# Kernel tuning notes

Hardware: AMD Instinct MI355X
Metric: run time of the kernel (lower is better)

Reference implementation:

```python
import jax, jax.numpy as jnp
import numpy as np

DIM = 1024
HEADS = 16
HEAD_DIM = DIM // HEADS
HIDDEN = 4 * DIM
EPS = 1e-5


def layer_norm(x, g, b):
    mu = jnp.mean(x, axis=-1, keepdims=True)
    var = jnp.var(x, axis=-1, keepdims=True)
    return (x - mu) * jax.lax.rsqrt(var + EPS) * g + b


def setup_inputs() -> dict:
    key = jax.random.key(0)
    ks = jax.random.split(key, 8)
    B, N, C = 2, 2048, DIM
    # xavier-uniform-ish scales
    s_qkv = float(np.sqrt(6.0 / (C + 3 * C)))
    s_proj = float(np.sqrt(6.0 / (C + C)))
    s_fc1 = float(np.sqrt(6.0 / (C + HIDDEN)))
    return {
        "x": jax.random.normal(ks[0], (B, N, C), jnp.float32),
        "w_qkv": jax.random.uniform(ks[1], (3 * C, C), jnp.float32, -s_qkv, s_qkv),
        "w_proj": jax.random.uniform(ks[2], (C, C), jnp.float32, -s_proj, s_proj),
        "b_proj": jnp.zeros((C,), jnp.float32),
        "ln1_g": jnp.ones((C,), jnp.float32),
        "ln1_b": jnp.zeros((C,), jnp.float32),
        "ln2_g": jnp.ones((C,), jnp.float32),
        "ln2_b": jnp.zeros((C,), jnp.float32),
        "w_fc1": jax.random.uniform(ks[3], (HIDDEN, C), jnp.float32, -s_fc1, s_fc1),
        "b_fc1": jnp.zeros((HIDDEN,), jnp.float32),
        "w_fc2": jax.random.uniform(ks[4], (C, HIDDEN), jnp.float32, -s_fc1, s_fc1),
        "b_fc2": jnp.zeros((C,), jnp.float32),
    }


def attention(x, w_qkv, w_proj, b_proj):
    B, N, C = x.shape
    qkv = x @ w_qkv.T  # [B,N,3C]
    qkv = qkv.reshape(B, N, 3, HEADS, HEAD_DIM).transpose(2, 0, 3, 1, 4)
    q, k, v = qkv[0], qkv[1], qkv[2]  # [B,H,N,hd]
    scale = HEAD_DIM ** -0.5
    attn = jnp.einsum("bhqd,bhkd->bhqk", q, k) * scale
    attn = jax.nn.softmax(attn, axis=-1)
    out = jnp.einsum("bhqk,bhkd->bhqd", attn, v)  # [B,H,N,hd]
    out = out.transpose(0, 2, 1, 3).reshape(B, N, C)
    return out @ w_proj.T + b_proj


def reference(x, w_qkv, w_proj, b_proj, ln1_g, ln1_b, ln2_g, ln2_b, w_fc1, b_fc1, w_fc2, b_fc2):
    x = x + attention(layer_norm(x, ln1_g, ln1_b), w_qkv, w_proj, b_proj)
    h = layer_norm(x, ln2_g, ln2_b)
    h = jax.nn.gelu(h @ w_fc1.T + b_fc1, approximate=False)
    x = x + (h @ w_fc2.T + b_fc2)
    return x
```

## Files before the change

kernel.cpp:

```cpp
#include <hip/hip_runtime.h>
#include <hip/hip_bf16.h>
#include <math.h>

typedef __bf16 bf16;
typedef __attribute__((ext_vector_type(8))) __bf16 bf16x8;
typedef __attribute__((ext_vector_type(4))) __bf16 bf16x4;
typedef __attribute__((ext_vector_type(4))) float f32x4;

#define DEV static __device__ __forceinline__

typedef const void __attribute__((address_space(1)))* gptr_t;
typedef void __attribute__((address_space(3)))* lptr_t;

DEV void async16(const void* g, void* l) {
  __builtin_amdgcn_global_load_lds((gptr_t)g, (lptr_t)l, 16, 0, 0);
}

DEV void wg_barrier() {
  __builtin_amdgcn_sched_barrier(0);
  __builtin_amdgcn_s_barrier();
  __builtin_amdgcn_sched_barrier(0);
}

__global__ __launch_bounds__(256) void f2b4_kernel(const float* __restrict__ s0,
                                                   const float* __restrict__ s1,
                                                   const float* __restrict__ s2,
                                                   const float* __restrict__ s3,
                                                   bf16* __restrict__ d0, bf16* __restrict__ d1,
                                                   bf16* __restrict__ d2, bf16* __restrict__ d3,
                                                   int n0, int n1, int n2, int n3) {
  int i = (blockIdx.x * 256 + threadIdx.x) * 4;
  const float* s;
  bf16* d;
  int off;
  if (i < n0) { s = s0; d = d0; off = i; }
  else if (i < n0 + n1) { s = s1; d = d1; off = i - n0; }
  else if (i < n0 + n1 + n2) { s = s2; d = d2; off = i - n0 - n1; }
  else if (i < n0 + n1 + n2 + n3) { s = s3; d = d3; off = i - n0 - n1 - n2; }
  else return;
  float4 v = *(const float4*)(s + off);
  d[off + 0] = (bf16)v.x;
  d[off + 1] = (bf16)v.y;
  d[off + 2] = (bf16)v.z;
  d[off + 3] = (bf16)v.w;
}

__global__ __launch_bounds__(256) void ln_kernel(const float* __restrict__ in,
                                                 const float* __restrict__ g,
                                                 const float* __restrict__ b,
                                                 bf16* __restrict__ out) {
  const int row = blockIdx.x;
  const int tid = threadIdx.x;
  float4 v = ((const float4*)(in + (size_t)row * 1024))[tid];
  float s = v.x + v.y + v.z + v.w;
  float s2 = v.x * v.x + v.y * v.y + v.z * v.z + v.w * v.w;
#pragma unroll
  for (int off = 1; off < 64; off <<= 1) {
    s += __shfl_xor(s, off);
    s2 += __shfl_xor(s2, off);
  }
  __shared__ float red[8];
  int w = tid >> 6, lane = tid & 63;
  if (lane == 0) { red[w] = s; red[4 + w] = s2; }
  __syncthreads();
  s = red[0] + red[1] + red[2] + red[3];
  s2 = red[4] + red[5] + red[6] + red[7];
  const float mean = s * (1.f / 1024.f);
  const float var = s2 * (1.f / 1024.f) - mean * mean;
  const float rstd = rsqrtf(var + 1e-5f);
  float4 gv = ((const float4*)g)[tid];
  float4 bv = ((const float4*)b)[tid];
  bf16* orow = out + (size_t)row * 1024 + tid * 4;
  orow[0] = (bf16)((v.x - mean) * rstd * gv.x + bv.x);
  orow[1] = (bf16)((v.y - mean) * rstd * gv.y + bv.y);
  orow[2] = (bf16)((v.z - mean) * rstd * gv.z + bv.z);
  orow[3] = (bf16)((v.w - mean) * rstd * gv.w + bv.w);
}

template <int EPI>
__global__ __launch_bounds__(512, 2) void gemm256(const bf16* __restrict__ A,
                                                  const bf16* __restrict__ B,
                                                  bf16* __restrict__ outb,
                                                  const float* __restrict__ bias,
                                                  int M, int N, int K, int gridN) {
  __shared__ bf16 As[2][256 * 64];
  __shared__ bf16 Bs[2][256 * 64];
  const int nwg = gridDim.x;
  const int bid = blockIdx.x;
  const int swz = (bid & 7) * (nwg >> 3) + (bid >> 3);
  const int bx = swz % gridN, by = swz / gridN;
  const int brow = by * 256, bcol = bx * 256;
  const int tid = threadIdx.x;
  const int lane = tid & 63, wid = tid >> 6;
  const int wm = wid >> 2, wn = wid & 3;
  const int lr = lane & 15, lk4 = lane >> 4;
  const int strow = tid >> 3, stc = tid & 7;
  const int NT = K >> 6;
  f32x4 acc[8][4] = {};

#define STAGE(tt, bb)                                                                   \
  {                                                                                     \
    const int k0_ = (tt)*64;                                                            \
    _Pragma("unroll") for (int s_ = 0; s_ < 4; ++s_) {                                  \
      const int r_ = s_ * 64 + strow;                                                   \
      const int g_ = (stc ^ (strow & 7)) * 8;                                           \
      async16(A + (size_t)(brow + r_) * K + k0_ + g_, &As[bb][r_ * 64 + stc * 8]);      \
      async16(B + (size_t)(bcol + r_) * K + k0_ + g_, &Bs[bb][r_ * 64 + stc * 8]);      \
    }                                                                                   \
  }

  STAGE(0, 0);
  STAGE(1, 1);
  asm volatile("s_waitcnt vmcnt(8)" ::: "memory");
  wg_barrier();

  for (int t = 0; t < NT; ++t) {
    const int cur = t & 1;
    bf16x8 af[8][2], bfr[4][2];
#pragma unroll
    for (int m = 0; m < 8; ++m)
#pragma unroll
      for (int kk = 0; kk < 2; ++kk) {
        const int row = wm * 128 + m * 16 + lr;
        const int kc = kk * 4 + lk4;
        af[m][kk] = *(const bf16x8*)&As[cur][row * 64 + ((kc ^ (row & 7)) * 8)];
      }
#pragma unroll
    for (int n = 0; n < 4; ++n)
#pragma unroll
      for (int kk = 0; kk < 2; ++kk) {
        const int row = wn * 64 + n * 16 + lr;
        const int kc = kk * 4 + lk4;
        bfr[n][kk] = *(const bf16x8*)&Bs[cur][row * 64 + ((kc ^ (row & 7)) * 8)];
      }
    asm volatile("s_waitcnt lgkmcnt(0)" ::: "memory");
    wg_barrier();
    if (t + 2 < NT) STAGE(t + 2, cur);
    __builtin_amdgcn_s_setprio(1);
#pragma unroll
    for (int m = 0; m < 8; ++m)
#pragma unroll
      for (int n = 0; n < 4; ++n) {
        acc[m][n] = __builtin_amdgcn_mfma_f32_16x16x32_bf16(af[m][0], bfr[n][0], acc[m][n], 0, 0, 0);
        acc[m][n] = __builtin_amdgcn_mfma_f32_16x16x32_bf16(af[m][1], bfr[n][1], acc[m][n], 0, 0, 0);
      }
    __builtin_amdgcn_s_setprio(0);
    if (t + 1 < NT) {
      if (t + 2 < NT) {
        asm volatile("s_waitcnt vmcnt(8)" ::: "memory");
      } else {
        asm volatile("s_waitcnt vmcnt(0)" ::: "memory");
      }
      wg_barrier();
    }
  }
#undef STAGE
  const int r0 = brow + wm * 128 + lk4 * 4;
  const int c0 = bcol + wn * 64 + lr;
  float bias_v[4];
  if (EPI == 1) {
#pragma unroll
    for (int n = 0; n < 4; ++n) bias_v[n] = bias[c0 + n * 16];
  }
#pragma unroll
  for (int m = 0; m < 8; ++m)
#pragma unroll
    for (int n = 0; n < 4; ++n)
#pragma unroll
      for (int j = 0; j < 4; ++j) {
        const int r = r0 + m * 16 + j;
        const int c = c0 + n * 16;
        float v = acc[m][n][j];
        if (EPI == 1) {
          v += bias_v[n];
          v = 0.5f * v * (1.0f + erff(v * 0.70710678118654752f));
        }
        outb[(size_t)r * N + c] = (bf16)v;
      }
}

__global__ __launch_bounds__(512, 2) void gemm128(const bf16* __restrict__ A,
                                                  const bf16* __restrict__ B,
                                                  float* __restrict__ outf,
                                                  const float* __restrict__ bias,
                                                  const float* __restrict__ resid,
                                                  int M, int N, int K, int gridN) {
  __shared__ bf16 As[2][128 * 64];
  __shared__ bf16 Bs[2][128 * 64];
  const int nwg = gridDim.x;
  const int bid = blockIdx.x;
  const int swz = (bid & 7) * (nwg >> 3) + (bid >> 3);
  const int bx = swz % gridN, by = swz / gridN;
  const int brow = by * 128, bcol = bx * 128;
  const int tid = threadIdx.x;
  const int lane = tid & 63, wid = tid >> 6;
  const int wk = wid & 1, wn = (wid >> 1) & 1, wm = wid >> 2;
  const int lr = lane & 15, lk4 = lane >> 4;
  const int strow = tid >> 3, stc = tid & 7;
  const int NT = K >> 6;
  f32x4 acc[4][4] = {};

#define STAGE1(tt, bb)                                                                  \
  {                                                                                     \
    const int k0_ = (tt)*64;                                                            \
    _Pragma("unroll") for (int s_ = 0; s_ < 2; ++s_) {                                  \
      const int r_ = s_ * 64 + strow;                                                   \
      const int g_ = (stc ^ (strow & 7)) * 8;                                           \
      async16(A + (size_t)(brow + r_) * K + k0_ + g_, &As[bb][r_ * 64 + stc * 8]);      \
      async16(B + (size_t)(bcol + r_) * K + k0_ + g_, &Bs[bb][r_ * 64 + stc * 8]);      \
    }                                                                                   \
  }

  STAGE1(0, 0);
  STAGE1(1, 1);
  asm volatile("s_waitcnt vmcnt(4)" ::: "memory");
  wg_barrier();

  const int kc = wk * 4 + lk4;
  for (int t = 0; t < NT; ++t) {
    const int cur = t & 1;
    bf16x8 af[4], bfr[4];
#pragma unroll
    for (int m = 0; m < 4; ++m) {
      const int row = wm * 64 + m * 16 + lr;
      af[m] = *(const bf16x8*)&As[cur][row * 64 + ((kc ^ (row & 7)) * 8)];
    }
#pragma unroll
    for (int n = 0; n < 4; ++n) {
      const int row = wn * 64 + n * 16 + lr;
      bfr[n] = *(const bf16x8*)&Bs[cur][row * 64 + ((kc ^ (row & 7)) * 8)];
    }
    asm volatile("s_waitcnt lgkmcnt(0)" ::: "memory");
    wg_barrier();
    if (t + 2 < NT) STAGE1(t + 2, cur);
    __builtin_amdgcn_s_setprio(1);
#pragma unroll
    for (int m = 0; m < 4; ++m)
#pragma unroll
      for (int n = 0; n < 4; ++n)
        acc[m][n] = __builtin_amdgcn_mfma_f32_16x16x32_bf16(af[m], bfr[n], acc[m][n], 0, 0, 0);
    __builtin_amdgcn_s_setprio(0);
    if (t + 1 < NT) {
      if (t + 2 < NT) {
        asm volatile("s_waitcnt vmcnt(4)" ::: "memory");
      } else {
        asm volatile("s_waitcnt vmcnt(0)" ::: "memory");
      }
      wg_barrier();
    }
  }
#undef STAGE1
  __syncthreads();
  {
    const int r = wm * 2 + wn;
    float* reg = (r < 2) ? ((float*)&As[0][0] + r * 4096)
                         : ((float*)&Bs[0][0] + (r - 2) * 4096);
    if (wk == 1) {
#pragma unroll
      for (int m = 0; m < 4; ++m)
#pragma unroll
        for (int n = 0; n < 4; ++n)
#pragma unroll
          for (int j = 0; j < 4; ++j)
            reg[(m * 16 + n * 4 + j) * 64 + lane] = acc[m][n][j];
    }
    __syncthreads();
    if (wk == 0) {
      const int r0 = brow + wm * 64 + lk4 * 4;
      const int c0 = bcol + wn * 64 + lr;
#pragma unroll
      for (int m = 0; m < 4; ++m)
#pragma unroll
        for (int n = 0; n < 4; ++n) {
          const int c = c0 + n * 16;
          const float bv = bias[c];
#pragma unroll
          for (int j = 0; j < 4; ++j) {
            const int rr = r0 + m * 16 + j;
            float v = acc[m][n][j] + reg[(m * 16 + n * 4 + j) * 64 + lane];
            outf[(size_t)rr * N + c] = v + bv + resid[(size_t)rr * N + c];
          }
        }
    }
  }
}

__global__ __launch_bounds__(512, 4) void flash_kernel(const bf16* __restrict__ qkv,
                                                       bf16* __restrict__ out) {
  const int bid = blockIdx.x;
  const int swz = (bid & 7) * 64 + (bid >> 3);
  const int qt = swz & 15;
  const int bh = swz >> 4;
  const int b = bh >> 4, h = bh & 15;
  const int tid = threadIdx.x;
  const int lane = tid & 63, w = tid >> 6;
  const int lr = lane & 15, lk4 = lane >> 4;
  const bf16* Qp = qkv + (size_t)(b * 2048) * 3072 + h * 64;
  const bf16* Kp = Qp + 1024;
  const bf16* Vp = Qp + 2048;
  __shared__ bf16 Ks[2][64 * 64];
  __shared__ bf16 VTs[2][64 * 64];
  __shared__ bf16 Ps[128 * 64 + 4096];
  const int qw0 = qt * 128 + w * 16;
  const float SC = 0.125f * 1.44269504f;
  const float THRU = 8.0f / SC;
  bf16x8 qf[2];
#pragma unroll
  for (int kk = 0; kk < 2; ++kk)
    qf[kk] = *(const bf16x8*)(Qp + (size_t)(qw0 + lr) * 3072 + kk * 32 + lk4 * 8);
  f32x4 o[4] = {};
  float mrun = -1e30f, lrun = 0.f;
  const int sr = tid >> 3, sc8 = tid & 7;
  const int vd = tid & 63, vkc = (tid >> 6) * 8;
  const int vch = tid >> 6;
  const int prow = (w * 16 + lr) * 64;
  bf16 vv[8];
  async16(Kp + (size_t)sr * 3072 + (sc8 ^ (sr & 7)) * 8, &Ks[0][sr * 64 + sc8 * 8]);
#pragma unroll
  for (int j = 0; j < 8; ++j) vv[j] = Vp[(size_t)(vkc + j) * 3072 + vd];
  {
    bf16x8 a;
#pragma unroll
    for (int j = 0; j < 8; ++j) a[j] = vv[j];
    *(bf16x8*)&VTs[0][vd * 64 + ((vch ^ (vd & 7)) * 8)] = a;
  }
  __syncthreads();
  for (int t = 0; t < 32; ++t) {
    const int cur = t & 1, nxt = cur ^ 1;
    if (t < 31) {
      const size_t kv0n = (size_t)(t + 1) * 64;
      async16(Kp + (kv0n + sr) * 3072 + (sc8 ^ (sr & 7)) * 8, &Ks[nxt][sr * 64 + sc8 * 8]);
#pragma unroll
      for (int j = 0; j < 8; ++j) vv[j] = Vp[(kv0n + vkc + j) * 3072 + vd];
    }
    f32x4 st[4] = {};
    __builtin_amdgcn_s_setprio(1);
#pragma unroll
    for (int n = 0; n < 4; ++n)
#pragma unroll
      for (int kk = 0; kk < 2; ++kk) {
        bf16x8 kf = *(const bf16x8*)&Ks[cur][(n * 16 + lr) * 64 + (((kk * 4 + lk4) ^ (lr & 7)) * 8)];
        st[n] = __builtin_amdgcn_mfma_f32_16x16x32_bf16(kf, qf[kk], st[n], 0, 0, 0);
      }
    __builtin_amdgcn_s_setprio(0);
    float m01 = fmaxf(fmaxf(st[0][0], st[0][1]), fmaxf(st[0][2], st[0][3]));
    float m23 = fmaxf(fmaxf(st[1][0], st[1][1]), fmaxf(st[1][2], st[1][3]));
    float m45 = fmaxf(fmaxf(st[2][0], st[2][1]), fmaxf(st[2][2], st[2][3]));
    float m67 = fmaxf(fmaxf(st[3][0], st[3][1]), fmaxf(st[3][2], st[3][3]));
    float mx = fmaxf(fmaxf(m01, m23), fmaxf(m45, m67));
    mx = fmaxf(mx, __shfl_xor(mx, 16));
    mx = fmaxf(mx, __shfl_xor(mx, 32));
    const bool skip = __all(mx <= mrun + THRU);
    const float mn = skip ? mrun : fmaxf(mrun, mx);
    const float mnS = mn * SC;
    float rs = 0.f;
#pragma unroll
    for (int n = 0; n < 4; ++n) {
      float p0 = exp2f(fmaf(st[n][0], SC, -mnS));
      float p1 = exp2f(fmaf(st[n][1], SC, -mnS));
      float p2 = exp2f(fmaf(st[n][2], SC, -mnS));
      float p3 = exp2f(fmaf(st[n][3], SC, -mnS));
      rs += (p0 + p1) + (p2 + p3);
      bf16x4 pk;
      pk[0] = (bf16)p0; pk[1] = (bf16)p1; pk[2] = (bf16)p2; pk[3] = (bf16)p3;
      *(bf16x4*)&Ps[prow + (((n * 2 + (lk4 >> 1)) ^ (lr & 7)) * 8) + (lk4 & 1) * 4] = pk;
    }
    rs += __shfl_xor(rs, 16);
    rs += __shfl_xor(rs, 32);
    if (!skip) {
      const float alpha = exp2f(fmaf(mrun, SC, -mnS));
      lrun = lrun * alpha + rs;
      mrun = mn;
#pragma unroll
      for (int c = 0; c < 4; ++c)
#pragma unroll
        for (int j = 0; j < 4; ++j) o[c][j] *= alpha;
    } else {
      lrun += rs;
    }
    bf16x8 pb[2];
#pragma unroll
    for (int kk = 0; kk < 2; ++kk)
      pb[kk] = *(const bf16x8*)&Ps[prow + (((kk * 4 + lk4) ^ (lr & 7)) * 8)];
    __builtin_amdgcn_s_setprio(1);
#pragma unroll
    for (int c = 0; c < 4; ++c)
#pragma unroll
      for (int kk = 0; kk < 2; ++kk) {
        bf16x8 vfr = *(const bf16x8*)&VTs[cur][(c * 16 + lr) * 64 + (((kk * 4 + lk4) ^ (lr & 7)) * 8)];
        o[c] = __builtin_amdgcn_mfma_f32_16x16x32_bf16(vfr, pb[kk], o[c], 0, 0, 0);
      }
    __builtin_amdgcn_s_setprio(0);
    if (t < 31) {
      bf16x8 a;
#pragma unroll
      for (int j = 0; j < 8; ++j) a[j] = vv[j];
      *(bf16x8*)&VTs[nxt][vd * 64 + ((vch ^ (vd & 7)) * 8)] = a;
    }
    __syncthreads();
  }
  const float inv = 1.f / lrun;
#pragma unroll
  for (int c = 0; c < 4; ++c) {
    bf16x4 ov;
#pragma unroll
    for (int j = 0; j < 4; ++j) ov[j] = (bf16)(o[c][j] * inv);
    *(bf16x4*)&out[(size_t)(b * 2048 + qw0 + lr) * 1024 + h * 64 + c * 16 + lk4 * 4] = ov;
  }
}

extern "C" void kernel_launch(void* const* d_in, const int* in_sizes, int n_in,
                              void* d_out, int out_size, void* d_ws, size_t ws_size,
                              hipStream_t stream) {
  const float* x      = (const float*)d_in[0];
  const float* w_qkv  = (const float*)d_in[1];
  const float* w_proj = (const float*)d_in[2];
  const float* b_proj = (const float*)d_in[3];
  const float* ln1_g  = (const float*)d_in[4];
  const float* ln1_b  = (const float*)d_in[5];
  const float* ln2_g  = (const float*)d_in[6];
  const float* ln2_b  = (const float*)d_in[7];
  const float* w_fc1  = (const float*)d_in[8];
  const float* b_fc1  = (const float*)d_in[9];
  const float* w_fc2  = (const float*)d_in[10];
  const float* b_fc2  = (const float*)d_in[11];

  char* W = (char*)d_ws;
  bf16* wqkvb = (bf16*)(W + 0);
  bf16* wprojb = (bf16*)(W + 6291456);
  bf16* wfc1b = (bf16*)(W + 8388608);
  bf16* wfc2b = (bf16*)(W + 16777216);
  bf16* xn    = (bf16*)(W + 25165824);
  bf16* qkvb  = (bf16*)(W + 33554432);
  bf16* attnb = (bf16*)(W + 58720256);
  float* x2   = (float*)(W + 67108864);
  bf16* hbuf  = (bf16*)(W + 83886080);
  float* outf = (float*)d_out;

  f2b4_kernel<<<12288, 256, 0, stream>>>(w_qkv, w_proj, w_fc1, w_fc2,
                                         wqkvb, wprojb, wfc1b, wfc2b,
                                         3145728, 1048576, 4194304, 4194304);

  ln_kernel<<<4096, 256, 0, stream>>>(x, ln1_g, ln1_b, xn);
  gemm256<0><<<192, 512, 0, stream>>>(xn, wqkvb, qkvb, nullptr, 4096, 3072, 1024, 12);
  flash_kernel<<<512, 512, 0, stream>>>(qkvb, attnb);
  gemm128<<<256, 512, 0, stream>>>(attnb, wprojb, x2, b_proj, x, 4096, 1024, 1024, 8);
  ln_kernel<<<4096, 256, 0, stream>>>(x2, ln2_g, ln2_b, xn);
  gemm256<1><<<256, 512, 0, stream>>>(xn, wfc1b, hbuf, b_fc1, 4096, 4096, 1024, 16);
  gemm128<<<256, 512, 0, stream>>>(hbuf, wfc2b, outf, b_fc2, x2, 4096, 1024, 4096, 8);
}
```

Measured before the change: 250.6 us.

## Store residual stream in bf16 and unroll flash loop with precomputed offsets

The intermediate residual x2 is now written as bf16 instead of fp32 by the attention projection GEMM. A new bf16-input layernorm reads it, and the final GEMM adds it back as the residual, which halves that buffer's traffic. The flash attention loop is also unrolled by two with compile-time buffer indices, precomputed LDS offsets and pointer-increment prefetch addressing, to cut integer address arithmetic. The cost is a loss of residual precision, since x2 is rounded to bf16 before the final add.

```diff
diff --git a/kernel.cpp b/kernel.cpp
--- a/kernel.cpp
+++ b/kernel.cpp
@@ -77,6 +77,40 @@
   orow[3] = (bf16)((v.w - mean) * rstd * gv.w + bv.w);
 }
 
+__global__ __launch_bounds__(256) void ln_kernel_b(const bf16* __restrict__ in,
+                                                   const float* __restrict__ g,
+                                                   const float* __restrict__ b,
+                                                   bf16* __restrict__ out) {
+  const int row = blockIdx.x;
+  const int tid = threadIdx.x;
+  bf16x4 vb = ((const bf16x4*)(in + (size_t)row * 1024))[tid];
+  float4 v;
+  v.x = (float)vb[0]; v.y = (float)vb[1]; v.z = (float)vb[2]; v.w = (float)vb[3];
+  float s = v.x + v.y + v.z + v.w;
+  float s2 = v.x * v.x + v.y * v.y + v.z * v.z + v.w * v.w;
+#pragma unroll
+  for (int off = 1; off < 64; off <<= 1) {
+    s += __shfl_xor(s, off);
+    s2 += __shfl_xor(s2, off);
+  }
+  __shared__ float red[8];
+  int w = tid >> 6, lane = tid & 63;
+  if (lane == 0) { red[w] = s; red[4 + w] = s2; }
+  __syncthreads();
+  s = red[0] + red[1] + red[2] + red[3];
+  s2 = red[4] + red[5] + red[6] + red[7];
+  const float mean = s * (1.f / 1024.f);
+  const float var = s2 * (1.f / 1024.f) - mean * mean;
+  const float rstd = rsqrtf(var + 1e-5f);
+  float4 gv = ((const float4*)g)[tid];
+  float4 bv = ((const float4*)b)[tid];
+  bf16* orow = out + (size_t)row * 1024 + tid * 4;
+  orow[0] = (bf16)((v.x - mean) * rstd * gv.x + bv.x);
+  orow[1] = (bf16)((v.y - mean) * rstd * gv.y + bv.y);
+  orow[2] = (bf16)((v.z - mean) * rstd * gv.z + bv.z);
+  orow[3] = (bf16)((v.w - mean) * rstd * gv.w + bv.w);
+}
+
 template <int EPI>
 __global__ __launch_bounds__(512, 2) void gemm256(const bf16* __restrict__ A,
                                                   const bf16* __restrict__ B,
@@ -179,11 +213,14 @@
       }
 }
 
+template <int EPI>
 __global__ __launch_bounds__(512, 2) void gemm128(const bf16* __restrict__ A,
                                                   const bf16* __restrict__ B,
+                                                  bf16* __restrict__ outb,
                                                   float* __restrict__ outf,
                                                   const float* __restrict__ bias,
-                                                  const float* __restrict__ resid,
+                                                  const float* __restrict__ residf,
+                                                  const bf16* __restrict__ residb,
                                                   int M, int N, int K, int gridN) {
   __shared__ bf16 As[2][128 * 64];
   __shared__ bf16 Bs[2][128 * 64];
@@ -277,8 +314,12 @@
 #pragma unroll
           for (int j = 0; j < 4; ++j) {
             const int rr = r0 + m * 16 + j;
-            float v = acc[m][n][j] + reg[(m * 16 + n * 4 + j) * 64 + lane];
-            outf[(size_t)rr * N + c] = v + bv + resid[(size_t)rr * N + c];
+            float v = acc[m][n][j] + reg[(m * 16 + n * 4 + j) * 64 + lane] + bv;
+            if (EPI == 0) {
+              outb[(size_t)rr * N + c] = (bf16)(v + residf[(size_t)rr * N + c]);
+            } else {
+              outf[(size_t)rr * N + c] = v + (float)residb[(size_t)rr * N + c];
+            }
           }
         }
     }
@@ -314,91 +355,107 @@
   const int vd = tid & 63, vkc = (tid >> 6) * 8;
   const int vch = tid >> 6;
   const int prow = (w * 16 + lr) * 64;
+  int koff[4][2], pw[4], pr[2];
+#pragma unroll
+  for (int n = 0; n < 4; ++n) {
+#pragma unroll
+    for (int kk = 0; kk < 2; ++kk)
+      koff[n][kk] = (n * 16 + lr) * 64 + (((kk * 4 + lk4) ^ (lr & 7)) * 8);
+    pw[n] = prow + (((n * 2 + (lk4 >> 1)) ^ (lr & 7)) * 8) + (lk4 & 1) * 4;
+  }
+#pragma unroll
+  for (int kk = 0; kk < 2; ++kk) pr[kk] = prow + (((kk * 4 + lk4) ^ (lr & 7)) * 8);
+  const int kso = sc8 ^ (sr & 7);
+  const int kdst = sr * 64 + sc8 * 8;
+  const int vdst = vd * 64 + ((vch ^ (vd & 7)) * 8);
+  const bf16* Kst = Kp + (size_t)64 * 3072;
+  const bf16* Vst = Vp + (size_t)64 * 3072;
+  const int ksrc = sr * 3072 + kso * 8;
+  const int vsrc = vkc * 3072 + vd;
   bf16 vv[8];
-  async16(Kp + (size_t)sr * 3072 + (sc8 ^ (sr & 7)) * 8, &Ks[0][sr * 64 + sc8 * 8]);
-#pragma unroll
-  for (int j = 0; j < 8; ++j) vv[j] = Vp[(size_t)(vkc + j) * 3072 + vd];
+  async16(Kp + ksrc, &Ks[0][kdst]);
+#pragma unroll
+  for (int j = 0; j < 8; ++j) vv[j] = Vp[vsrc + j * 3072];
   {
     bf16x8 a;
 #pragma unroll
     for (int j = 0; j < 8; ++j) a[j] = vv[j];
-    *(bf16x8*)&VTs[0][vd * 64 + ((vch ^ (vd & 7)) * 8)] = a;
+    *(bf16x8*)&VTs[0][vdst] = a;
   }
   __syncthreads();
-  for (int t = 0; t < 32; ++t) {
-    const int cur = t & 1, nxt = cur ^ 1;
-    if (t < 31) {
-      const size_t kv0n = (size_t)(t + 1) * 64;
-      async16(Kp + (kv0n + sr) * 3072 + (sc8 ^ (sr & 7)) * 8, &Ks[nxt][sr * 64 + sc8 * 8]);
-#pragma unroll
-      for (int j = 0; j < 8; ++j) vv[j] = Vp[(kv0n + vkc + j) * 3072 + vd];
-    }
-    f32x4 st[4] = {};
-    __builtin_amdgcn_s_setprio(1);
-#pragma unroll
-    for (int n = 0; n < 4; ++n)
-#pragma unroll
-      for (int kk = 0; kk < 2; ++kk) {
-        bf16x8 kf = *(const bf16x8*)&Ks[cur][(n * 16 + lr) * 64 + (((kk * 4 + lk4) ^ (lr & 7)) * 8)];
-        st[n] = __builtin_amdgcn_mfma_f32_16x16x32_bf16(kf, qf[kk], st[n], 0, 0, 0);
-      }
-    __builtin_amdgcn_s_setprio(0);
-    float m01 = fmaxf(fmaxf(st[0][0], st[0][1]), fmaxf(st[0][2], st[0][3]));
-    float m23 = fmaxf(fmaxf(st[1][0], st[1][1]), fmaxf(st[1][2], st[1][3]));
-    float m45 = fmaxf(fmaxf(st[2][0], st[2][1]), fmaxf(st[2][2], st[2][3]));
-    float m67 = fmaxf(fmaxf(st[3][0], st[3][1]), fmaxf(st[3][2], st[3][3]));
-    float mx = fmaxf(fmaxf(m01, m23), fmaxf(m45, m67));
-    mx = fmaxf(mx, __shfl_xor(mx, 16));
-    mx = fmaxf(mx, __shfl_xor(mx, 32));
-    const bool skip = __all(mx <= mrun + THRU);
-    const float mn = skip ? mrun : fmaxf(mrun, mx);
-    const float mnS = mn * SC;
-    float rs = 0.f;
-#pragma unroll
-    for (int n = 0; n < 4; ++n) {
-      float p0 = exp2f(fmaf(st[n][0], SC, -mnS));
-      float p1 = exp2f(fmaf(st[n][1], SC, -mnS));
-      float p2 = exp2f(fmaf(st[n][2], SC, -mnS));
-      float p3 = exp2f(fmaf(st[n][3], SC, -mnS));
-      rs += (p0 + p1) + (p2 + p3);
-      bf16x4 pk;
-      pk[0] = (bf16)p0; pk[1] = (bf16)p1; pk[2] = (bf16)p2; pk[3] = (bf16)p3;
-      *(bf16x4*)&Ps[prow + (((n * 2 + (lk4 >> 1)) ^ (lr & 7)) * 8) + (lk4 & 1) * 4] = pk;
-    }
-    rs += __shfl_xor(rs, 16);
-    rs += __shfl_xor(rs, 32);
-    if (!skip) {
-      const float alpha = exp2f(fmaf(mrun, SC, -mnS));
-      lrun = lrun * alpha + rs;
-      mrun = mn;
-#pragma unroll
-      for (int c = 0; c < 4; ++c)
-#pragma unroll
-        for (int j = 0; j < 4; ++j) o[c][j] *= alpha;
-    } else {
-      lrun += rs;
-    }
-    bf16x8 pb[2];
-#pragma unroll
-    for (int kk = 0; kk < 2; ++kk)
-      pb[kk] = *(const bf16x8*)&Ps[prow + (((kk * 4 + lk4) ^ (lr & 7)) * 8)];
-    __builtin_amdgcn_s_setprio(1);
-#pragma unroll
-    for (int c = 0; c < 4; ++c)
-#pragma unroll
-      for (int kk = 0; kk < 2; ++kk) {
-        bf16x8 vfr = *(const bf16x8*)&VTs[cur][(c * 16 + lr) * 64 + (((kk * 4 + lk4) ^ (lr & 7)) * 8)];
-        o[c] = __builtin_amdgcn_mfma_f32_16x16x32_bf16(vfr, pb[kk], o[c], 0, 0, 0);
-      }
-    __builtin_amdgcn_s_setprio(0);
-    if (t < 31) {
-      bf16x8 a;
-#pragma unroll
-      for (int j = 0; j < 8; ++j) a[j] = vv[j];
-      *(bf16x8*)&VTs[nxt][vd * 64 + ((vch ^ (vd & 7)) * 8)] = a;
-    }
-    __syncthreads();
-  }
+
+#define FTILE(CUR, PREF)                                                                \
+  {                                                                                     \
+    if (PREF) {                                                                         \
+      async16(Kst + ksrc, &Ks[CUR ^ 1][kdst]);                                          \
+      _Pragma("unroll") for (int j = 0; j < 8; ++j) vv[j] = Vst[vsrc + j * 3072];       \
+    }                                                                                   \
+    f32x4 st[4] = {};                                                                   \
+    __builtin_amdgcn_s_setprio(1);                                                      \
+    _Pragma("unroll") for (int n = 0; n < 4; ++n)                                       \
+      _Pragma("unroll") for (int kk = 0; kk < 2; ++kk) {                                \
+        bf16x8 kf = *(const bf16x8*)&Ks[CUR][koff[n][kk]];                              \
+        st[n] = __builtin_amdgcn_mfma_f32_16x16x32_bf16(kf, qf[kk], st[n], 0, 0, 0);    \
+      }                                                                                 \
+    __builtin_amdgcn_s_setprio(0);                                                      \
+    float m01 = fmaxf(fmaxf(st[0][0], st[0][1]), fmaxf(st[0][2], st[0][3]));            \
+    float m23 = fmaxf(fmaxf(st[1][0], st[1][1]), fmaxf(st[1][2], st[1][3]));            \
+    float m45 = fmaxf(fmaxf(st[2][0], st[2][1]), fmaxf(st[2][2], st[2][3]));            \
+    float m67 = fmaxf(fmaxf(st[3][0], st[3][1]), fmaxf(st[3][2], st[3][3]));            \
+    float mx = fmaxf(fmaxf(m01, m23), fmaxf(m45, m67));                                 \
+    mx = fmaxf(mx, __shfl_xor(mx, 16));                                                 \
+    mx = fmaxf(mx, __shfl_xor(mx, 32));                                                 \
+    const bool skip = __all(mx <= mrun + THRU);                                         \
+    const float mn = skip ? mrun : fmaxf(mrun, mx);                                     \
+    const float mnS = mn * SC;                                                          \
+    float rs = 0.f;                                                                     \
+    _Pragma("unroll") for (int n = 0; n < 4; ++n) {                                     \
+      float p0 = exp2f(fmaf(st[n][0], SC, -mnS));                                       \
+      float p1 = exp2f(fmaf(st[n][1], SC, -mnS));                                       \
+      float p2 = exp2f(fmaf(st[n][2], SC, -mnS));                                       \
+      float p3 = exp2f(fmaf(st[n][3], SC, -mnS));                                       \
+      rs += (p0 + p1) + (p2 + p3);                                                      \
+      bf16x4 pk;                                                                        \
+      pk[0] = (bf16)p0; pk[1] = (bf16)p1; pk[2] = (bf16)p2; pk[3] = (bf16)p3;           \
+      *(bf16x4*)&Ps[pw[n]] = pk;                                                        \
+    }                                                                                   \
+    rs += __shfl_xor(rs, 16);                                                           \
+    rs += __shfl_xor(rs, 32);                                                           \
+    if (!skip) {                                                                        \
+      const float alpha = exp2f(fmaf(mrun, SC, -mnS));                                  \
+      lrun = lrun * alpha + rs;                                                         \
+      mrun = mn;                                                                        \
+      _Pragma("unroll") for (int c = 0; c < 4; ++c)                                     \
+        _Pragma("unroll") for (int j = 0; j < 4; ++j) o[c][j] *= alpha;                 \
+    } else {                                                                            \
+      lrun += rs;                                                                       \
+    }                                                                                   \
+    bf16x8 pb[2];                                                                       \
+    _Pragma("unroll") for (int kk = 0; kk < 2; ++kk)                                    \
+      pb[kk] = *(const bf16x8*)&Ps[pr[kk]];                                             \
+    __builtin_amdgcn_s_setprio(1);                                                      \
+    _Pragma("unroll") for (int c = 0; c < 4; ++c)                                       \
+      _Pragma("unroll") for (int kk = 0; kk < 2; ++kk) {                                \
+        bf16x8 vfr = *(const bf16x8*)&VTs[CUR][koff[c][kk]];                            \
+        o[c] = __builtin_amdgcn_mfma_f32_16x16x32_bf16(vfr, pb[kk], o[c], 0, 0, 0);     \
+      }                                                                                 \
+    __builtin_amdgcn_s_setprio(0);                                                      \
+    if (PREF) {                                                                         \
+      bf16x8 a;                                                                         \
+      _Pragma("unroll") for (int j = 0; j < 8; ++j) a[j] = vv[j];                       \
+      *(bf16x8*)&VTs[CUR ^ 1][vdst] = a;                                                \
+      Kst += (size_t)64 * 3072;                                                         \
+      Vst += (size_t)64 * 3072;                                                         \
+    }                                                                                   \
+    __syncthreads();                                                                    \
+  }
+
+  for (int tt = 0; tt < 16; ++tt) {
+    FTILE(0, true);
+    FTILE(1, (tt < 15));
+  }
+#undef FTILE
+
   const float inv = 1.f / lrun;
 #pragma unroll
   for (int c = 0; c < 4; ++c) {
@@ -433,7 +490,7 @@
   bf16* xn    = (bf16*)(W + 25165824);
   bf16* qkvb  = (bf16*)(W + 33554432);
   bf16* attnb = (bf16*)(W + 58720256);
-  float* x2   = (float*)(W + 67108864);
+  bf16* x2b   = (bf16*)(W + 67108864);
   bf16* hbuf  = (bf16*)(W + 83886080);
   float* outf = (float*)d_out;
 
@@ -444,8 +501,10 @@
   ln_kernel<<<4096, 256, 0, stream>>>(x, ln1_g, ln1_b, xn);
   gemm256<0><<<192, 512, 0, stream>>>(xn, wqkvb, qkvb, nullptr, 4096, 3072, 1024, 12);
   flash_kernel<<<512, 512, 0, stream>>>(qkvb, attnb);
-  gemm128<<<256, 512, 0, stream>>>(attnb, wprojb, x2, b_proj, x, 4096, 1024, 1024, 8);
-  ln_kernel<<<4096, 256, 0, stream>>>(x2, ln2_g, ln2_b, xn);
+  gemm128<0><<<256, 512, 0, stream>>>(attnb, wprojb, x2b, nullptr, b_proj, x, nullptr,
+                                      4096, 1024, 1024, 8);
+  ln_kernel_b<<<4096, 256, 0, stream>>>(x2b, ln2_g, ln2_b, xn);
   gemm256<1><<<256, 512, 0, stream>>>(xn, wfc1b, hbuf, b_fc1, 4096, 4096, 1024, 16);
-  gemm128<<<256, 512, 0, stream>>>(hbuf, wfc2b, outf, b_fc2, x2, 4096, 1024, 4096, 8);
-}
+  gemm128<1><<<256, 512, 0, stream>>>(hbuf, wfc2b, nullptr, outf, b_fc2, nullptr, x2b,
+                                      4096, 1024, 4096, 8);
+}
```

Result: faster. 245.4 us (median of 2 runs) (-2.1%).
